# Performance work log

Measured on AMD Instinct MI355X. Metric: run time of the kernel, lower is better.

Reference implementation:

```python
import jax, jax.numpy as jnp
import numpy as np
import math

B, T, D, H = 2, 4096, 2048, 16
HD = D // H  # 128
OFFSET = -math.log(math.sqrt(D)) + 1e-6  # q_offset == k_offset in the original


def setup_inputs() -> dict:
    key = jax.random.key(0)
    ks = jax.random.split(key, 7)
    s = 1.0 / np.sqrt(D).astype(np.float32)  # keep exp() in a sane range
    return {
        "hidden_states": jax.random.normal(ks[0], (B, T, D), jnp.float32),
        "Wq": jax.random.normal(ks[1], (D, D), jnp.float32) * s,
        "Wk": jax.random.normal(ks[2], (D, D), jnp.float32) * s,
        "Wv": jax.random.normal(ks[3], (D, D), jnp.float32) * s,
        "Wo": jax.random.normal(ks[4], (D, D), jnp.float32) * s,
        "Fq": jax.random.normal(ks[5], (D, D), jnp.float32) * s,  # q feature map
        "Fk": jax.random.normal(ks[6], (D, D), jnp.float32) * s,  # k feature map
    }


def _split_heads(x):
    # [B, T, D] -> [B, H, T, HD]
    return x.reshape(B, T, H, HD).transpose(0, 2, 1, 3)


def reference(hidden_states, Wq, Wk, Wv, Wo, Fq, Fk):
    q = hidden_states @ Wq
    k = hidden_states @ Wk
    v = hidden_states @ Wv
    # Performer-style positive feature maps
    q_prime = jnp.exp(q @ Fq + OFFSET)
    k_prime = jnp.exp(k @ Fk + OFFSET)
    q_p = _split_heads(q_prime)   # [B,H,T,HD]
    k_p = _split_heads(k_prime)
    v_h = _split_heads(v)
    # causal_attention1: q_t^T (k_t v_t^T) == (q_t . k_t) * v_t, then cumsum over T.
    # Equivalent to the original [B,H,T,HD,HD] outer-product + cumsum, without
    # materializing the huge intermediate.
    dot = jnp.einsum("bhtd,bhtd->bht", q_p, k_p)           # [B,H,T]
    att_raw = jnp.cumsum(dot[..., None] * v_h, axis=2)      # [B,H,T,HD]
    attn = att_raw / k_p                                    # att_norm = k_prime
    # merge heads: [B,H,T,HD] -> [B,T,D]
    attn = attn.transpose(0, 2, 1, 3).reshape(B, T, D)
    return attn @ Wo
```

## Files before the change

### kernel.cpp

```cpp
#include <hip/hip_runtime.h>
#include <hip/hip_bf16.h>
#include <cmath>

constexpr int Bc = 2, Tc = 4096, Dc = 2048, Hc = 16, HDc = 128;
constexpr int Mrows = Bc * Tc;
constexpr int NCHUNK = 32, CHUNK = 128;
constexpr int BHT = Bc * Hc * Tc;

__device__ __forceinline__ unsigned short f2bf(float x) {
  union { float f; unsigned int u; } v; v.f = x;
  unsigned int r = v.u + 0x7FFFu + ((v.u >> 16) & 1u);
  return (unsigned short)(r >> 16);
}
__device__ __forceinline__ float bf2f(unsigned short u) {
  union { unsigned int i; float f; } v; v.i = ((unsigned int)u) << 16;
  return v.f;
}

typedef __attribute__((ext_vector_type(8))) short bf16x8;
typedef __attribute__((ext_vector_type(4))) float f32x4;

__device__ __forceinline__ void gload16(const unsigned short* g, unsigned short* l) {
  __builtin_amdgcn_global_load_lds(
      (const __attribute__((address_space(1))) void*)(const void*)g,
      (__attribute__((address_space(3))) void*)(void*)l,
      16, 0, 0);
}

__global__ void cvt_bf16(const float* __restrict__ in, unsigned short* __restrict__ outp) {
  size_t i = ((size_t)blockIdx.x * 256 + threadIdx.x) * 4;
  float4 f = *(const float4*)(in + i);
  ushort4 u;
  u.x = f2bf(f.x); u.y = f2bf(f.y); u.z = f2bf(f.z); u.w = f2bf(f.w);
  *(ushort4*)(outp + i) = u;
}

__global__ void add_bf16(unsigned short* __restrict__ dst, const unsigned short* __restrict__ src) {
  size_t i = ((size_t)blockIdx.x * 256 + threadIdx.x) * 8;
  bf16x8 a = *(const bf16x8*)(dst + i);
  bf16x8 b = *(const bf16x8*)(src + i);
#pragma unroll
  for (int j = 0; j < 8; ++j)
    a[j] = (short)f2bf(bf2f((unsigned short)a[j]) + bf2f((unsigned short)b[j]));
  *(bf16x8*)(dst + i) = a;
}

__global__ void prep6(const float* __restrict__ W0, unsigned short* __restrict__ T0,
                      const float* __restrict__ W1, unsigned short* __restrict__ T1,
                      const float* __restrict__ W2, unsigned short* __restrict__ T2,
                      const float* __restrict__ W3, unsigned short* __restrict__ T3,
                      const float* __restrict__ C4, unsigned short* __restrict__ O4,
                      const float* __restrict__ C5, unsigned short* __restrict__ O5) {
  const int z = blockIdx.z;
  const int n0 = blockIdx.x * 32, k0 = blockIdx.y * 32;
  const int tx = threadIdx.x & 31, ty = threadIdx.x >> 5;
  if (z >= 4) {
    const float* in = (z == 4) ? C4 : C5;
    unsigned short* op = (z == 4) ? O4 : O5;
#pragma unroll
    for (int i = 0; i < 4; ++i) {
      size_t idx = (size_t)(k0 + ty + 8 * i) * Dc + n0 + tx;
      op[idx] = f2bf(in[idx]);
    }
    return;
  }
  const float* W; unsigned short* Wt;
  switch (z) {
    case 0: W = W0; Wt = T0; break;
    case 1: W = W1; Wt = T1; break;
    case 2: W = W2; Wt = T2; break;
    default: W = W3; Wt = T3; break;
  }
  __shared__ float tile[32][33];
#pragma unroll
  for (int i = 0; i < 4; ++i)
    tile[ty + 8 * i][tx] = W[(size_t)(k0 + ty + 8 * i) * Dc + n0 + tx];
  __syncthreads();
#pragma unroll
  for (int i = 0; i < 4; ++i)
    Wt[(size_t)(n0 + ty + 8 * i) * Dc + k0 + tx] = f2bf(tile[tx][ty + 8 * i]);
}

template <int EPI>
__global__ __launch_bounds__(512, 2) void gemm8(
    const unsigned short* __restrict__ A,
    const unsigned short* __restrict__ Bt,
    void* __restrict__ C0, void* __restrict__ C1, void* __restrict__ C2,
    int M, int N, int lda, int ldc, float eoff) {
  constexpr int K = 2048;
  constexpr int NT = K / 64;
  extern __shared__ unsigned short lds[];

  const int tid = threadIdx.x;
  const int lane = tid & 63;
  const int wave = tid >> 6;
  const int wm = wave >> 2;
  const int wn = wave & 3;

  const int nbn = N >> 8;
  const int nwg = (M >> 8) * nbn;
  const int bidx = (int)blockIdx.x;
  const int wgid = (bidx & 7) * (nwg >> 3) + (bidx >> 3);
  const int bm = wgid / nbn;
  const int bn = wgid % nbn;

  const int srow = tid >> 2;
  const int scolL = (tid & 3) << 3;
  const int scolG = scolL ^ ((srow & 6) << 2);
  const unsigned short* gA = A + (size_t)(bm * 256 + srow) * lda + scolG;
  const unsigned short* gB = Bt + (size_t)(bn * 256 + srow) * K + scolG;
  const int sstage = srow * 32 + scolL;
  const size_t arstep = (size_t)128 * lda;
  const size_t brstep = (size_t)128 * K;

  const int fr = lane & 15;
  const int fko = ((lane >> 4) << 3) ^ ((lane & 6) << 2);
  const int aoff = (wm * 128 + fr) * 32 + fko;
  const int boff = 16384 + (wn * 64 + fr) * 32 + fko;

  f32x4 acc[8][4] = {};

  gload16(gA,               lds + sstage);
  gload16(gA + arstep,      lds + sstage + 4096);
  gload16(gB,               lds + 16384 + sstage);
  gload16(gB + brstep,      lds + 16384 + sstage + 4096);
  gload16(gA + 32,          lds + 8192 + sstage);
  gload16(gA + 32 + arstep, lds + 8192 + sstage + 4096);
  gload16(gB + 32,          lds + 24576 + sstage);
  gload16(gB + 32 + brstep, lds + 24576 + sstage + 4096);
  asm volatile("s_waitcnt vmcnt(4)" ::: "memory");
  __builtin_amdgcn_s_barrier();

#define PH_MFMA(MOFF)                                                         \
  __builtin_amdgcn_s_barrier();                                               \
  asm volatile("s_waitcnt lgkmcnt(0)" ::: "memory");                          \
  __builtin_amdgcn_s_setprio(1);                                              \
  _Pragma("unroll")                                                           \
  for (int mi = 0; mi < 4; ++mi)                                              \
    _Pragma("unroll")                                                         \
    for (int ni = 0; ni < 4; ++ni)                                            \
      acc[(MOFF) + mi][ni] = __builtin_amdgcn_mfma_f32_16x16x32_bf16(         \
          af[mi], bfv[ni], acc[(MOFF) + mi][ni], 0, 0, 0);                    \
  __builtin_amdgcn_s_setprio(0);

#define TILE8(RB, WB, TN)                                                     \
  {                                                                           \
    const unsigned short* sA = gA + (TN) * 64;                                \
    const unsigned short* sB = gB + (TN) * 64;                                \
    bf16x8 af[4], bfv[4];                                                     \
                               \
    _Pragma("unroll")                                                         \
    for (int mi = 0; mi < 4; ++mi)                                            \
      af[mi] = *(const bf16x8*)(lds + (RB) + aoff + mi * 512);                \
    _Pragma("unroll")                                                         \
    for (int ni = 0; ni < 4; ++ni)                                            \
      bfv[ni] = *(const bf16x8*)(lds + (RB) + boff + ni * 512);               \
    gload16(sA,          lds + (WB) + sstage);                                \
    gload16(sA + arstep, lds + (WB) + sstage + 4096);                         \
    PH_MFMA(0)                                                                \
    __builtin_amdgcn_s_barrier();                                             \
                   \
    _Pragma("unroll")                                                         \
    for (int mi = 0; mi < 4; ++mi)                                            \
      af[mi] = *(const bf16x8*)(lds + (RB) + aoff + (4 + mi) * 512);          \
    gload16(sB,          lds + (WB) + 16384 + sstage);                        \
    gload16(sB + brstep, lds + (WB) + 16384 + sstage + 4096);                 \
    PH_MFMA(4)                                                                \
    asm volatile("s_waitcnt vmcnt(4)" ::: "memory");   \
    __builtin_amdgcn_s_barrier();                                             \
                               \
    _Pragma("unroll")                                                         \
    for (int mi = 0; mi < 4; ++mi)                                            \
      af[mi] = *(const bf16x8*)(lds + (RB) + 8192 + aoff + mi * 512);         \
    _Pragma("unroll")                                                         \
    for (int ni = 0; ni < 4; ++ni)                                            \
      bfv[ni] = *(const bf16x8*)(lds + (RB) + 8192 + boff + ni * 512);        \
    gload16(sA + 32,          lds + (WB) + 8192 + sstage);                    \
    gload16(sA + 32 + arstep, lds + (WB) + 8192 + sstage + 4096);             \
    PH_MFMA(0)                                                                \
    __builtin_amdgcn_s_barrier();                                             \
                               \
    _Pragma("unroll")                                                         \
    for (int mi = 0; mi < 4; ++mi)                                            \
      af[mi] = *(const bf16x8*)(lds + (RB) + 8192 + aoff + (4 + mi) * 512);   \
    gload16(sB + 32,          lds + (WB) + 24576 + sstage);                   \
    gload16(sB + 32 + brstep, lds + (WB) + 24576 + sstage + 4096);            \
    PH_MFMA(4)                                                                \
    asm volatile("s_waitcnt vmcnt(4)" ::: "memory"); \
    __builtin_amdgcn_s_barrier();                                             \
  }

  for (int vv = 0; vv < NT; vv += 2) {
    TILE8(0,     32768, vv + 1)
    TILE8(32768, 0,     (vv + 2) & (NT - 1))
  }
#undef TILE8
#undef PH_MFMA

  const int fq = lane >> 4;
  const int crow = bm * 256 + wm * 128;
  if constexpr (EPI == 5) {
    const int seg = bn >> 3;
    if (seg == 0) {
      float s2[8][4];
#pragma unroll
      for (int mi = 0; mi < 8; ++mi)
#pragma unroll
        for (int ii = 0; ii < 4; ++ii) {
          float t = 0.f;
#pragma unroll
          for (int ni = 0; ni < 4; ++ni)
            t += __expf(acc[mi][ni][ii] + 2.f * eoff);
          s2[mi][ii] = t;
        }
#pragma unroll
      for (int m = 1; m < 16; m <<= 1)
#pragma unroll
        for (int mi = 0; mi < 8; ++mi)
#pragma unroll
          for (int ii = 0; ii < 4; ++ii)
            s2[mi][ii] += __shfl_xor(s2[mi][ii], m);
      const int h = (bn & 7) * 2 + (wn >> 1);
      const int part = wn & 1;
      float* dp = (float*)C0 + (size_t)part * BHT;
#pragma unroll
      for (int u = 0; u < 2; ++u) {
        const int idx = fr * 2 + u;
        const int mi = idx >> 2, ii = idx & 3;
        const int r = crow + mi * 16 + fq * 4 + ii;
        const int b = r >> 12, t = r & (Tc - 1);
        dp[((size_t)(b * Hc + h)) * Tc + t] = s2[mi][ii];
      }
    } else {
      unsigned short* outp = (unsigned short*)(seg == 1 ? C1 : C2);
      const int ccol = (bn & 7) * 256 + wn * 64 + fr;
#pragma unroll
      for (int mi = 0; mi < 8; ++mi)
#pragma unroll
        for (int ni = 0; ni < 4; ++ni)
#pragma unroll
          for (int ii = 0; ii < 4; ++ii) {
            const int r = crow + mi * 16 + fq * 4 + ii;
            const int c = ccol + ni * 16;
            float vv = acc[mi][ni][ii];
            if (seg == 1) vv = __expf(vv + eoff);
            outp[(size_t)r * ldc + c] = f2bf(vv);
          }
    }
  } else {
    const int ccol = bn * 256 + wn * 64 + fr;
#pragma unroll
    for (int mi = 0; mi < 8; ++mi)
#pragma unroll
      for (int ni = 0; ni < 4; ++ni)
#pragma unroll
        for (int ii = 0; ii < 4; ++ii) {
          const int r = crow + mi * 16 + fq * 4 + ii;
          const int c = ccol + ni * 16;
          ((float*)C0)[(size_t)r * ldc + c] = acc[mi][ni][ii];
        }
  }
}

__global__ __launch_bounds__(256, 2) void gemmW(
    const unsigned short* __restrict__ A0, const unsigned short* __restrict__ B0,
    unsigned short* __restrict__ C0,
    const unsigned short* __restrict__ A1, const unsigned short* __restrict__ B1,
    unsigned short* __restrict__ C1) {
  constexpr int K = 2048, N = 2048;
  constexpr int NT = K / 32;
  constexpr int BM = 128, BN = 128;
  constexpr int ASLAB = BM * 32, BSLAB = BN * 32, BUF = ASLAB + BSLAB;
  constexpr int SROWS = 64;
  extern __shared__ unsigned short lds[];

  const unsigned short* A = blockIdx.y ? A1 : A0;
  const unsigned short* Bt = blockIdx.y ? B1 : B0;
  unsigned short* C = blockIdx.y ? C1 : C0;

  const int tid = threadIdx.x;
  const int lane = tid & 63;
  const int wave = tid >> 6;
  const int wm = wave >> 1, wn = wave & 1;

  const int nbn = N / BN;
  const int nwg = (2048 / BM) * nbn;
  const int bidx = (int)blockIdx.x;
  const int wgid = (bidx & 7) * (nwg >> 3) + (bidx >> 3);
  const int bm = wgid / nbn;
  const int bn = wgid % nbn;

  const int srow = tid >> 2;
  const int scolL = (tid & 3) << 3;
  const int scolG = scolL ^ ((srow & 6) << 2);
  const unsigned short* gA = A + (size_t)(bm * BM + srow) * K + scolG;
  const unsigned short* gB = Bt + (size_t)(bn * BN + srow) * K + scolG;
  const int sstage = srow * 32 + scolL;
  const size_t rstep = (size_t)SROWS * K;

  const int fr = lane & 15;
  const int fko = ((lane >> 4) << 3) ^ ((lane & 6) << 2);
  const int aoff = (wm * 64 + fr) * 32 + fko;
  const int boff = ASLAB + (wn * 64 + fr) * 32 + fko;

  f32x4 acc[4][4] = {};

#pragma unroll
  for (int t = 0; t < 3; ++t) {
    const unsigned short* sA = gA + t * 32;
    const unsigned short* sB = gB + t * 32;
    unsigned short* dst = lds + t * BUF;
    gload16(sA,         dst + sstage);
    gload16(sA + rstep, dst + sstage + SROWS * 32);
    gload16(sB,         dst + ASLAB + sstage);
    gload16(sB + rstep, dst + ASLAB + sstage + SROWS * 32);
  }
  asm volatile("s_waitcnt vmcnt(8)" ::: "memory");
  __builtin_amdgcn_s_barrier();

  for (int v = 0; v < NT; ++v) {
    const int rb = (v & 3) * BUF;
    const int wb = ((v + 3) & 3) * BUF;
    const int tn = (v + 3) & (NT - 1);
    const unsigned short* srcA = gA + tn * 32;
    const unsigned short* srcB = gB + tn * 32;

    bf16x8 af[4], bfv[4];
#pragma unroll
    for (int mi = 0; mi < 4; ++mi)
      af[mi] = *(const bf16x8*)(lds + rb + aoff + mi * 512);
#pragma unroll
    for (int ni = 0; ni < 4; ++ni)
      bfv[ni] = *(const bf16x8*)(lds + rb + boff + ni * 512);

    gload16(srcA,         lds + wb + sstage);
    gload16(srcA + rstep, lds + wb + sstage + SROWS * 32);
    gload16(srcB,         lds + wb + ASLAB + sstage);
    gload16(srcB + rstep, lds + wb + ASLAB + sstage + SROWS * 32);

    __builtin_amdgcn_s_setprio(1);
#pragma unroll
    for (int mi = 0; mi < 4; ++mi)
#pragma unroll
      for (int ni = 0; ni < 4; ++ni)
        acc[mi][ni] = __builtin_amdgcn_mfma_f32_16x16x32_bf16(af[mi], bfv[ni], acc[mi][ni], 0, 0, 0);
    __builtin_amdgcn_s_setprio(0);

    asm volatile("s_waitcnt vmcnt(8)" ::: "memory");
    __builtin_amdgcn_s_barrier();
  }

  const int fq = lane >> 4;
#pragma unroll
  for (int mi = 0; mi < 4; ++mi)
#pragma unroll
    for (int ni = 0; ni < 4; ++ni)
#pragma unroll
      for (int ii = 0; ii < 4; ++ii) {
        const int r = bm * BM + wm * 64 + mi * 16 + fq * 4 + ii;
        const int c = bn * BN + wn * 64 + ni * 16 + fr;
        C[(size_t)r * N + c] = f2bf(acc[mi][ni][ii]);
      }
}

__global__ void scan_chunks2(const float* __restrict__ dotP,
                             const unsigned short* __restrict__ v,
                             float* __restrict__ dotb,
                             float* __restrict__ chks) {
  __shared__ float dt[CHUNK];
  const int bid = blockIdx.x;
  const int c = bid & (NCHUNK - 1);
  const int bh = bid >> 5;
  const int b = bh >> 4, h = bh & 15;
  const int d = threadIdx.x;
  const int t0 = c * CHUNK;

  const size_t di = (size_t)bh * Tc + t0 + d;
  float dv = dotP[di] + dotP[(size_t)BHT + di];
  dt[d] = dv;
  dotb[di] = dv;
  __syncthreads();

  const unsigned short* vp = v + ((size_t)(b * Tc + t0)) * Dc + h * HDc + d;
  float acc = 0.f;
  for (int t = 0; t < CHUNK; ++t)
    acc += dt[t] * bf2f(vp[(size_t)t * Dc]);
  chks[(size_t)bid * HDc + d] = acc;
}

__global__ void scan_final(const float* __restrict__ dotb,
                           const unsigned short* __restrict__ v,
                           const unsigned short* __restrict__ kp,
                           const float* __restrict__ chks,
                           unsigned short* __restrict__ attn) {
  int bid = blockIdx.x;
  int c = bid % NCHUNK, bh = bid / NCHUNK;
  int b = bh / Hc, h = bh % Hc;
  int d = threadIdx.x;
  float acc = 0.f;
  for (int cc = 0; cc < c; ++cc)
    acc += chks[((size_t)bh * NCHUNK + cc) * HDc + d];
  const float* dp = dotb + (size_t)bh * Tc + c * CHUNK;
  size_t base = ((size_t)(b * Tc + c * CHUNK)) * Dc + h * HDc + d;
  for (int t = 0; t < CHUNK; ++t) {
    size_t idx = base + (size_t)t * Dc;
    acc += dp[t] * bf2f(v[idx]);
    attn[idx] = f2bf(acc / bf2f(kp[idx]));
  }
}

extern "C" void kernel_launch(void* const* d_in, const int* in_sizes, int n_in,
                              void* d_out, int out_size, void* d_ws, size_t ws_size,
                              hipStream_t stream) {
  const float* hs = (const float*)d_in[0];
  const float* Wq = (const float*)d_in[1];
  const float* Wk = (const float*)d_in[2];
  const float* Wv = (const float*)d_in[3];
  const float* Wo = (const float*)d_in[4];
  const float* Fq = (const float*)d_in[5];
  const float* Fk = (const float*)d_in[6];
  float* out = (float*)d_out;

  const size_t MD = (size_t)Mrows * Dc;
  const size_t DD = (size_t)Dc * Dc;

  char* w = (char*)d_ws;
  size_t off = 0;
  auto take = [&](size_t bytes) -> void* {
    void* r = w + off;
    off += (bytes + 255) & ~(size_t)255;
    return r;
  };

  unsigned short* hs_bf = (unsigned short*)take(MD * 2);
  unsigned short* wq_bf = (unsigned short*)take(DD * 2);
  unsigned short* wtfq  = (unsigned short*)take(DD * 2);
  unsigned short* wk_bf = (unsigned short*)take(DD * 2);
  unsigned short* wtfk  = (unsigned short*)take(DD * 2);
  unsigned short* wcat  = (unsigned short*)take(3 * DD * 2);
  unsigned short* wto   = (unsigned short*)take(DD * 2);
  unsigned short* Kp    = (unsigned short*)take(MD * 2);
  unsigned short* Vbf   = (unsigned short*)take(MD * 2);
  float* dotP = (float*)take((size_t)2 * BHT * 4);
  float* dotb = (float*)take((size_t)BHT * 4);
  float* chks = (float*)take((size_t)Bc * Hc * NCHUNK * HDc * 4);

  unsigned short* attnbf = hs_bf;

  const float OFF = (float)(-0.5 * log(2048.0) + 1e-6);

  (void)hipFuncSetAttribute((const void*)gemm8<0>, hipFuncAttributeMaxDynamicSharedMemorySize, 131072);
  (void)hipFuncSetAttribute((const void*)gemm8<5>, hipFuncAttributeMaxDynamicSharedMemorySize, 131072);
  (void)hipFuncSetAttribute((const void*)gemmW,    hipFuncAttributeMaxDynamicSharedMemorySize, 65536);

  cvt_bf16<<<(int)(MD / 1024), 256, 0, stream>>>(hs, hs_bf);

  prep6<<<dim3(Dc / 32, Dc / 32, 6), 256, 0, stream>>>(
      Fq, wtfq, Fk, wtfk, Wv, wcat + 2 * DD, Wo, wto, Wq, wq_bf, Wk, wk_bf);

  gemmW<<<dim3(256, 2), 256, 65536, stream>>>(
      wtfq, wq_bf, wcat, wtfk, wk_bf, wcat + DD);

  add_bf16<<<(int)(DD / 2048), 256, 0, stream>>>(wcat, wcat + DD);

  const int fblocks = (Mrows / 256) * (6144 / 256);
  gemm8<5><<<fblocks, 512, 131072, stream>>>(
      hs_bf, wcat, dotP, Kp, Vbf, Mrows, 6144, Dc, Dc, OFF);

  scan_chunks2<<<Bc * Hc * NCHUNK, 128, 0, stream>>>(dotP, Vbf, dotb, chks);

  scan_final<<<Bc * Hc * NCHUNK, 128, 0, stream>>>(dotb, Vbf, Kp, chks, attnbf);

  const int gblocks = (Mrows / 256) * (Dc / 256);
  gemm8<0><<<gblocks, 512, 131072, stream>>>(
      attnbf, wto, out, nullptr, nullptr, Mrows, Dc, Dc, Dc, 0.f);
}
```

Measured before the change: 421.3 us.

## Replace 256x256 GEMM with 256x128 tile, K=32 triple-buffered pipeline

Rewrites the main GEMM kernel to use 256x128 output tiles with a K-step of 32 and a three-stage LDS ring buffer, instead of 256x256 tiles with K=64 double buffering. LDS use drops to 72KB and launch bounds rise so more workgroups can be resident per CU, and the grid doubles in size. The dot-product epilogue now writes four partial sums per head instead of two, and the scan kernel sums all four. The cost is lower arithmetic intensity per tile, more barriers per K, and extra global writes and reads for the partial sums.

```diff
diff --git a/kernel.cpp b/kernel.cpp
--- a/kernel.cpp
+++ b/kernel.cpp
@@ -82,13 +82,17 @@
 }
 
 template <int EPI>
-__global__ __launch_bounds__(512, 2) void gemm8(
+__global__ __launch_bounds__(512, 4) void gemmT(
     const unsigned short* __restrict__ A,
     const unsigned short* __restrict__ Bt,
     void* __restrict__ C0, void* __restrict__ C1, void* __restrict__ C2,
     int M, int N, int lda, int ldc, float eoff) {
   constexpr int K = 2048;
-  constexpr int NT = K / 64;
+  constexpr int NT = K / 32;
+  constexpr int BM = 256, BN = 128;
+  constexpr int ASLAB = BM * 32;
+  constexpr int BSLAB = BN * 32;
+  constexpr int BUF = ASLAB + BSLAB;
   extern __shared__ unsigned short lds[];
 
   const int tid = threadIdx.x;
@@ -97,7 +101,7 @@
   const int wm = wave >> 2;
   const int wn = wave & 3;
 
-  const int nbn = N >> 8;
+  const int nbn = N >> 7;
   const int nwg = (M >> 8) * nbn;
   const int bidx = (int)blockIdx.x;
   const int wgid = (bidx & 7) * (nwg >> 3) + (bidx >> 3);
@@ -107,110 +111,86 @@
   const int srow = tid >> 2;
   const int scolL = (tid & 3) << 3;
   const int scolG = scolL ^ ((srow & 6) << 2);
-  const unsigned short* gA = A + (size_t)(bm * 256 + srow) * lda + scolG;
-  const unsigned short* gB = Bt + (size_t)(bn * 256 + srow) * K + scolG;
+  const unsigned short* gA = A + (size_t)(bm * BM + srow) * lda + scolG;
+  const unsigned short* gB = Bt + (size_t)(bn * BN + srow) * K + scolG;
   const int sstage = srow * 32 + scolL;
   const size_t arstep = (size_t)128 * lda;
-  const size_t brstep = (size_t)128 * K;
 
   const int fr = lane & 15;
   const int fko = ((lane >> 4) << 3) ^ ((lane & 6) << 2);
   const int aoff = (wm * 128 + fr) * 32 + fko;
-  const int boff = 16384 + (wn * 64 + fr) * 32 + fko;
-
-  f32x4 acc[8][4] = {};
-
-  gload16(gA,               lds + sstage);
-  gload16(gA + arstep,      lds + sstage + 4096);
-  gload16(gB,               lds + 16384 + sstage);
-  gload16(gB + brstep,      lds + 16384 + sstage + 4096);
-  gload16(gA + 32,          lds + 8192 + sstage);
-  gload16(gA + 32 + arstep, lds + 8192 + sstage + 4096);
-  gload16(gB + 32,          lds + 24576 + sstage);
-  gload16(gB + 32 + brstep, lds + 24576 + sstage + 4096);
-  asm volatile("s_waitcnt vmcnt(4)" ::: "memory");
+  const int boff = ASLAB + (wn * 32 + fr) * 32 + fko;
+
+  f32x4 acc[8][2] = {};
+
+#pragma unroll
+  for (int t = 0; t < 2; ++t) {
+    const unsigned short* sA = gA + t * 32;
+    const unsigned short* sB = gB + t * 32;
+    unsigned short* dst = lds + t * BUF;
+    gload16(sA,          dst + sstage);
+    gload16(sA + arstep, dst + sstage + 4096);
+    gload16(sB,          dst + ASLAB + sstage);
+  }
+  asm volatile("s_waitcnt vmcnt(3)" ::: "memory");
   __builtin_amdgcn_s_barrier();
 
-#define PH_MFMA(MOFF)                                                         \
-  __builtin_amdgcn_s_barrier();                                               \
-  asm volatile("s_waitcnt lgkmcnt(0)" ::: "memory");                          \
-  __builtin_amdgcn_s_setprio(1);                                              \
-  _Pragma("unroll")                                                           \
-  for (int mi = 0; mi < 4; ++mi)                                              \
-    _Pragma("unroll")                                                         \
-    for (int ni = 0; ni < 4; ++ni)                                            \
-      acc[(MOFF) + mi][ni] = __builtin_amdgcn_mfma_f32_16x16x32_bf16(         \
-          af[mi], bfv[ni], acc[(MOFF) + mi][ni], 0, 0, 0);                    \
-  __builtin_amdgcn_s_setprio(0);
-
-#define TILE8(RB, WB, TN)                                                     \
-  {                                                                           \
-    const unsigned short* sA = gA + (TN) * 64;                                \
-    const unsigned short* sB = gB + (TN) * 64;                                \
-    bf16x8 af[4], bfv[4];                                                     \
-                               \
-    _Pragma("unroll")                                                         \
-    for (int mi = 0; mi < 4; ++mi)                                            \
-      af[mi] = *(const bf16x8*)(lds + (RB) + aoff + mi * 512);                \
-    _Pragma("unroll")                                                         \
-    for (int ni = 0; ni < 4; ++ni)                                            \
-      bfv[ni] = *(const bf16x8*)(lds + (RB) + boff + ni * 512);               \
-    gload16(sA,          lds + (WB) + sstage);                                \
-    gload16(sA + arstep, lds + (WB) + sstage + 4096);                         \
-    PH_MFMA(0)                                                                \
-    __builtin_amdgcn_s_barrier();                                             \
-                   \
-    _Pragma("unroll")                                                         \
-    for (int mi = 0; mi < 4; ++mi)                                            \
-      af[mi] = *(const bf16x8*)(lds + (RB) + aoff + (4 + mi) * 512);          \
-    gload16(sB,          lds + (WB) + 16384 + sstage);                        \
-    gload16(sB + brstep, lds + (WB) + 16384 + sstage + 4096);                 \
-    PH_MFMA(4)                                                                \
-    asm volatile("s_waitcnt vmcnt(4)" ::: "memory");   \
-    __builtin_amdgcn_s_barrier();                                             \
-                               \
-    _Pragma("unroll")                                                         \
-    for (int mi = 0; mi < 4; ++mi)                                            \
-      af[mi] = *(const bf16x8*)(lds + (RB) + 8192 + aoff + mi * 512);         \
-    _Pragma("unroll")                                                         \
-    for (int ni = 0; ni < 4; ++ni)                                            \
-      bfv[ni] = *(const bf16x8*)(lds + (RB) + 8192 + boff + ni * 512);        \
-    gload16(sA + 32,          lds + (WB) + 8192 + sstage);                    \
-    gload16(sA + 32 + arstep, lds + (WB) + 8192 + sstage + 4096);             \
-    PH_MFMA(0)                                                                \
-    __builtin_amdgcn_s_barrier();                                             \
-                               \
-    _Pragma("unroll")                                                         \
-    for (int mi = 0; mi < 4; ++mi)                                            \
-      af[mi] = *(const bf16x8*)(lds + (RB) + 8192 + aoff + (4 + mi) * 512);   \
-    gload16(sB + 32,          lds + (WB) + 24576 + sstage);                   \
-    gload16(sB + 32 + brstep, lds + (WB) + 24576 + sstage + 4096);            \
-    PH_MFMA(4)                                                                \
-    asm volatile("s_waitcnt vmcnt(4)" ::: "memory"); \
-    __builtin_amdgcn_s_barrier();                                             \
-  }
-
-  for (int vv = 0; vv < NT; vv += 2) {
-    TILE8(0,     32768, vv + 1)
-    TILE8(32768, 0,     (vv + 2) & (NT - 1))
-  }
-#undef TILE8
-#undef PH_MFMA
+  int rb = 0;
+  for (int v = 0; v < NT; ++v) {
+    int wb = rb + 2 * BUF; if (wb >= 3 * BUF) wb -= 3 * BUF;
+    const int tn = (v + 2) & (NT - 1);
+    const unsigned short* srcA = gA + tn * 32;
+    const unsigned short* srcB = gB + tn * 32;
+
+    bf16x8 af[4], bfv[2];
+    bfv[0] = *(const bf16x8*)(lds + rb + boff);
+    bfv[1] = *(const bf16x8*)(lds + rb + boff + 512);
+#pragma unroll
+    for (int mi = 0; mi < 4; ++mi)
+      af[mi] = *(const bf16x8*)(lds + rb + aoff + mi * 512);
+
+    gload16(srcA,          lds + wb + sstage);
+    gload16(srcA + arstep, lds + wb + sstage + 4096);
+    gload16(srcB,          lds + wb + ASLAB + sstage);
+
+    __builtin_amdgcn_s_setprio(1);
+#pragma unroll
+    for (int mi = 0; mi < 4; ++mi) {
+      acc[mi][0] = __builtin_amdgcn_mfma_f32_16x16x32_bf16(af[mi], bfv[0], acc[mi][0], 0, 0, 0);
+      acc[mi][1] = __builtin_amdgcn_mfma_f32_16x16x32_bf16(af[mi], bfv[1], acc[mi][1], 0, 0, 0);
+    }
+    __builtin_amdgcn_s_setprio(0);
+
+#pragma unroll
+    for (int mi = 0; mi < 4; ++mi)
+      af[mi] = *(const bf16x8*)(lds + rb + aoff + (4 + mi) * 512);
+
+    __builtin_amdgcn_s_setprio(1);
+#pragma unroll
+    for (int mi = 0; mi < 4; ++mi) {
+      acc[4 + mi][0] = __builtin_amdgcn_mfma_f32_16x16x32_bf16(af[mi], bfv[0], acc[4 + mi][0], 0, 0, 0);
+      acc[4 + mi][1] = __builtin_amdgcn_mfma_f32_16x16x32_bf16(af[mi], bfv[1], acc[4 + mi][1], 0, 0, 0);
+    }
+    __builtin_amdgcn_s_setprio(0);
+
+    asm volatile("s_waitcnt vmcnt(3)" ::: "memory");
+    __builtin_amdgcn_s_barrier();
+
+    rb += BUF; if (rb == 3 * BUF) rb = 0;
+  }
 
   const int fq = lane >> 4;
-  const int crow = bm * 256 + wm * 128;
+  const int crow = bm * BM + wm * 128;
   if constexpr (EPI == 5) {
-    const int seg = bn >> 3;
+    const int seg = bn >> 4;
     if (seg == 0) {
       float s2[8][4];
 #pragma unroll
       for (int mi = 0; mi < 8; ++mi)
 #pragma unroll
         for (int ii = 0; ii < 4; ++ii) {
-          float t = 0.f;
-#pragma unroll
-          for (int ni = 0; ni < 4; ++ni)
-            t += __expf(acc[mi][ni][ii] + 2.f * eoff);
+          float t = __expf(acc[mi][0][ii] + 2.f * eoff)
+                  + __expf(acc[mi][1][ii] + 2.f * eoff);
           s2[mi][ii] = t;
         }
 #pragma unroll
@@ -220,9 +200,8 @@
 #pragma unroll
           for (int ii = 0; ii < 4; ++ii)
             s2[mi][ii] += __shfl_xor(s2[mi][ii], m);
-      const int h = (bn & 7) * 2 + (wn >> 1);
-      const int part = wn & 1;
-      float* dp = (float*)C0 + (size_t)part * BHT;
+      const int h = bn;
+      float* dp = (float*)C0 + (size_t)wn * BHT;
 #pragma unroll
       for (int u = 0; u < 2; ++u) {
         const int idx = fr * 2 + u;
@@ -233,11 +212,11 @@
       }
     } else {
       unsigned short* outp = (unsigned short*)(seg == 1 ? C1 : C2);
-      const int ccol = (bn & 7) * 256 + wn * 64 + fr;
+      const int ccol = (bn & 15) * BN + wn * 32 + fr;
 #pragma unroll
       for (int mi = 0; mi < 8; ++mi)
 #pragma unroll
-        for (int ni = 0; ni < 4; ++ni)
+        for (int ni = 0; ni < 2; ++ni)
 #pragma unroll
           for (int ii = 0; ii < 4; ++ii) {
             const int r = crow + mi * 16 + fq * 4 + ii;
@@ -248,11 +227,11 @@
           }
     }
   } else {
-    const int ccol = bn * 256 + wn * 64 + fr;
+    const int ccol = bn * BN + wn * 32 + fr;
 #pragma unroll
     for (int mi = 0; mi < 8; ++mi)
 #pragma unroll
-      for (int ni = 0; ni < 4; ++ni)
+      for (int ni = 0; ni < 2; ++ni)
 #pragma unroll
         for (int ii = 0; ii < 4; ++ii) {
           const int r = crow + mi * 16 + fq * 4 + ii;
@@ -376,7 +355,8 @@
   const int t0 = c * CHUNK;
 
   const size_t di = (size_t)bh * Tc + t0 + d;
-  float dv = dotP[di] + dotP[(size_t)BHT + di];
+  float dv = dotP[di] + dotP[(size_t)BHT + di]
+           + dotP[2 * (size_t)BHT + di] + dotP[3 * (size_t)BHT + di];
   dt[d] = dv;
   dotb[di] = dv;
   __syncthreads();
@@ -441,7 +421,7 @@
   unsigned short* wto   = (unsigned short*)take(DD * 2);
   unsigned short* Kp    = (unsigned short*)take(MD * 2);
   unsigned short* Vbf   = (unsigned short*)take(MD * 2);
-  float* dotP = (float*)take((size_t)2 * BHT * 4);
+  float* dotP = (float*)take((size_t)4 * BHT * 4);
   float* dotb = (float*)take((size_t)BHT * 4);
   float* chks = (float*)take((size_t)Bc * Hc * NCHUNK * HDc * 4);
 
@@ -449,8 +429,8 @@
 
   const float OFF = (float)(-0.5 * log(2048.0) + 1e-6);
 
-  (void)hipFuncSetAttribute((const void*)gemm8<0>, hipFuncAttributeMaxDynamicSharedMemorySize, 131072);
-  (void)hipFuncSetAttribute((const void*)gemm8<5>, hipFuncAttributeMaxDynamicSharedMemorySize, 131072);
+  (void)hipFuncSetAttribute((const void*)gemmT<0>, hipFuncAttributeMaxDynamicSharedMemorySize, 73728);
+  (void)hipFuncSetAttribute((const void*)gemmT<5>, hipFuncAttributeMaxDynamicSharedMemorySize, 73728);
   (void)hipFuncSetAttribute((const void*)gemmW,    hipFuncAttributeMaxDynamicSharedMemorySize, 65536);
 
   cvt_bf16<<<(int)(MD / 1024), 256, 0, stream>>>(hs, hs_bf);
@@ -463,15 +443,15 @@
 
   add_bf16<<<(int)(DD / 2048), 256, 0, stream>>>(wcat, wcat + DD);
 
-  const int fblocks = (Mrows / 256) * (6144 / 256);
-  gemm8<5><<<fblocks, 512, 131072, stream>>>(
+  const int fblocks = (Mrows / 256) * (6144 / 128);
+  gemmT<5><<<fblocks, 512, 73728, stream>>>(
       hs_bf, wcat, dotP, Kp, Vbf, Mrows, 6144, Dc, Dc, OFF);
 
   scan_chunks2<<<Bc * Hc * NCHUNK, 128, 0, stream>>>(dotP, Vbf, dotb, chks);
 
   scan_final<<<Bc * Hc * NCHUNK, 128, 0, stream>>>(dotb, Vbf, Kp, chks, attnbf);
 
-  const int gblocks = (Mrows / 256) * (Dc / 256);
-  gemm8<0><<<gblocks, 512, 131072, stream>>>(
+  const int gblocks = (Mrows / 256) * (Dc / 128);
+  gemmT<0><<<gblocks, 512, 73728, stream>>>(
       attnbf, wto, out, nullptr, nullptr, Mrows, Dc, Dc, Dc, 0.f);
 }
```

Result: slower. 464.9 us (+10.3%).
